# Kernel optimization log

Measured on AMD Instinct MI355X. Metric: run time of the kernel, lower is better.

## Reference

```python
import jax, jax.numpy as jnp
from jax import lax
import numpy as np

ALPHA, BETA, DECAY, GAMMA = 0.9, 0.1, 0.9, 0.5
KW = 5  # temporal_window


def setup_inputs() -> dict:
    key = jax.random.key(0)
    k1, k2 = jax.random.split(key)
    B, T, F = 128, 128, 2048
    x = jax.random.normal(k1, (B, T, F), dtype=jnp.float32)
    init_threshold = jnp.array(1.0, dtype=jnp.float32)
    conv_w = jax.random.normal(k2, (1, 1, KW), dtype=jnp.float32) * 0.2  # Conv1d(1,1,KW) weight
    conv_b = jnp.zeros((1,), dtype=jnp.float32)
    spatial_attn = jnp.array([1.0], dtype=jnp.float32)
    return {"x": x, "init_threshold": init_threshold, "conv_w": conv_w,
            "conv_b": conv_b, "spatial_attn": spatial_attn}


def _forward(x, init_threshold, conv_w, conv_b, spatial_attn):
    B, T, F = x.shape
    # --- temporal encoding: Conv1d(1,1,KW,'same') along time, per (batch,feature) ---
    xt = jnp.transpose(x, (0, 2, 1)).reshape(B * F, 1, T)  # [B*F,1,T]
    conv = lax.conv_general_dilated(xt, conv_w, window_strides=(1,), padding='SAME',
                                    dimension_numbers=('NCH', 'OIH', 'NCH'))
    conv = conv + conv_b[None, :, None]
    x = jnp.transpose(conv.reshape(B, F, T), (0, 2, 1))  # [B,T,F]
    # --- spatial attention ---
    w = jax.nn.sigmoid(spatial_attn * x.mean(axis=1, keepdims=True))  # [B,1,F]
    x = x * (1.0 + GAMMA * w)
    # --- LIF recurrence over time ---
    mem0 = jnp.zeros((B, F), dtype=x.dtype)
    thr0 = jnp.broadcast_to(init_threshold, (B, F)).astype(x.dtype)
    hist0 = jnp.zeros((B, 3, F), dtype=x.dtype)
    pi = jnp.float32(np.pi)

    def step(carry, xt):
        mem, thr, hist = carry
        mem = DECAY * mem + xt
        spike = 0.5 * (jnp.arctan(pi * (mem - thr) / 2) / pi + 0.5)  # multi_atan surrogate
        hist = jnp.concatenate([hist[:, 1:], spike[:, None]], axis=1)  # [B,3,F]
        avg = hist.mean(axis=1)  # [B,F]
        new_thr = ALPHA * thr + (1.0 - ALPHA) * init_threshold + BETA * avg
        mem = mem - spike * lax.stop_gradient(new_thr)
        return (mem, new_thr, hist), spike

    (mem, _, _), spikes = lax.scan(step, (mem0, thr0, hist0), jnp.transpose(x, (1, 0, 2)))
    return jnp.transpose(spikes, (1, 0, 2)), mem  # [B,T,F], [B,F]


def reference(x, init_threshold, conv_w, conv_b, spatial_attn):
    return _forward(x, init_threshold, conv_w, conv_b, spatial_attn)
```

## Files before the change

### kernel.cpp

```cpp
#include <hip/hip_runtime.h>
#include <math.h>

constexpr int B = 128, T = 128, F = 2048, KW = 5;
#define ALPHA 0.9f
#define BETA  0.1f
#define DECAY 0.9f
#define GAMMA 0.5f

typedef float v2f __attribute__((ext_vector_type(2)));

__global__ __launch_bounds__(256, 2) void lif_fused_kernel(
    const float* __restrict__ x,
    const float* __restrict__ thr0p,
    const float* __restrict__ convw,
    const float* __restrict__ convb,
    const float* __restrict__ sattn,
    float* __restrict__ out)
{
    const int tid   = blockIdx.x * blockDim.x + threadIdx.x;
    const int fpair = tid & (F / 2 - 1);
    const int b     = tid >> 10;
    const int f     = fpair * 2;

    const float w0 = convw[0], w1 = convw[1], w2 = convw[2],
                w3 = convw[3], w4 = convw[4];
    const float cb   = convb[0];
    const float thr0 = thr0p[0];
    const float sa   = sattn[0];

    const float* xp = x + (size_t)b * T * F + f;

    v2f s0 = {0.f,0.f}, s1 = {0.f,0.f}, s2 = {0.f,0.f}, s3 = {0.f,0.f},
        s4 = {0.f,0.f}, s5 = {0.f,0.f}, s6 = {0.f,0.f}, s7 = {0.f,0.f};
#pragma unroll 2
    for (int t = 0; t < T; t += 8) {
        v2f v0 = *(const v2f*)(xp + (size_t)(t + 0) * F);
        v2f v1 = *(const v2f*)(xp + (size_t)(t + 1) * F);
        v2f v2 = *(const v2f*)(xp + (size_t)(t + 2) * F);
        v2f v3 = *(const v2f*)(xp + (size_t)(t + 3) * F);
        v2f v4 = *(const v2f*)(xp + (size_t)(t + 4) * F);
        v2f v5 = *(const v2f*)(xp + (size_t)(t + 5) * F);
        v2f v6 = *(const v2f*)(xp + (size_t)(t + 6) * F);
        v2f v7 = *(const v2f*)(xp + (size_t)(t + 7) * F);
        s0 += v0; s1 += v1; s2 += v2; s3 += v3;
        s4 += v4; s5 += v5; s6 += v6; s7 += v7;
    }
    v2f sx = ((s0 + s1) + (s2 + s3)) + ((s4 + s5) + (s6 + s7));

    v2f e0  = *(const v2f*)(xp);
    v2f e1  = *(const v2f*)(xp + (size_t)F);
    v2f em2 = *(const v2f*)(xp + (size_t)(T - 2) * F);
    v2f em1 = *(const v2f*)(xp + (size_t)(T - 1) * F);

    const float W = ((w0 + w1) + (w2 + w3)) + w4;
    v2f csum;
    csum.x = fmaf(W, sx.x, (float)T * cb)
           - (w3 + w4) * e0.x - w4 * e1.x - w0 * em2.x - (w0 + w1) * em1.x;
    csum.y = fmaf(W, sx.y, (float)T * cb)
           - (w3 + w4) * e0.y - w4 * e1.y - w0 * em2.y - (w0 + w1) * em1.y;

    v2f scale;
    {
        float zx = sa * (csum.x * (1.0f / (float)T));
        float zy = sa * (csum.y * (1.0f / (float)T));
        scale.x = 1.0f + GAMMA * (1.0f / (1.0f + expf(-zx)));
        scale.y = 1.0f + GAMMA * (1.0f / (1.0f + expf(-zy)));
    }

    const float PI  = 3.14159265358979323846f;
    const float thc = (1.0f - ALPHA) * thr0;

    v2f mem = {0.f, 0.f};
    v2f thr = {thr0, thr0};
    v2f h1 = {0.f, 0.f}, h2 = {0.f, 0.f};
    v2f a = {0.f, 0.f}, bb = {0.f, 0.f}, c = e0, d = e1;

    float* sp = out + (size_t)b * T * F + f;
    float* mp = out + (size_t)B * T * F + (size_t)b * F + f;

    auto lif_step = [&](int t, v2f e) {
        float cx = fmaf(w0, a.x, fmaf(w1, bb.x, fmaf(w2, c.x,
                   fmaf(w3, d.x, fmaf(w4, e.x, cb)))));
        float cy = fmaf(w0, a.y, fmaf(w1, bb.y, fmaf(w2, c.y,
                   fmaf(w3, d.y, fmaf(w4, e.y, cb)))));
        mem.x = fmaf(DECAY, mem.x, cx * scale.x);
        mem.y = fmaf(DECAY, mem.y, cy * scale.y);
        float sgx = PI * (mem.x - thr.x) * 0.5f;
        float sgy = PI * (mem.y - thr.y) * 0.5f;
        float spx = 0.5f * (atanf(sgx) * (1.0f / PI) + 0.5f);
        float spy = 0.5f * (atanf(sgy) * (1.0f / PI) + 0.5f);
        float avx = (h1.x + h2.x + spx) * (1.0f / 3.0f);
        float avy = (h1.y + h2.y + spy) * (1.0f / 3.0f);
        h1 = h2; h2.x = spx; h2.y = spy;
        thr.x = fmaf(ALPHA, thr.x, fmaf(BETA, avx, thc));
        thr.y = fmaf(ALPHA, thr.y, fmaf(BETA, avy, thc));
        mem.x = fmaf(-spx, thr.x, mem.x);
        mem.y = fmaf(-spy, thr.y, mem.y);
        v2f spv = {spx, spy};
        __builtin_nontemporal_store(spv, (v2f*)(sp + (size_t)t * F));
        a = bb; bb = c; c = d; d = e;
    };

    v2f A[8], Bv[8];

#define LOADG(buf, base)                                        \
    _Pragma("unroll")                                           \
    for (int j = 0; j < 8; ++j)                                 \
        buf[j] = *(const v2f*)(xp + (size_t)((base) + j) * F);

#define COMPUTE8(buf, t0)                                       \
    _Pragma("unroll")                                           \
    for (int j = 0; j < 8; ++j)                                 \
        lif_step((t0) + j, buf[j]);

    LOADG(A, 2);
    for (int p = 0; p < 7; ++p) {
        const int t0 = 16 * p;
        LOADG(Bv, t0 + 10);
        COMPUTE8(A, t0);
        LOADG(A, t0 + 18);
        COMPUTE8(Bv, t0 + 8);
    }
#pragma unroll
    for (int j = 0; j < 8; ++j) {
        if (j < 6) Bv[j] = *(const v2f*)(xp + (size_t)(122 + j) * F);
        else       Bv[j] = (v2f){0.f, 0.f};
    }
    COMPUTE8(A, 112);
    COMPUTE8(Bv, 120);

#undef LOADG
#undef COMPUTE8

    __builtin_nontemporal_store(mem, (v2f*)mp);
}

extern "C" void kernel_launch(void* const* d_in, const int* in_sizes, int n_in,
                              void* d_out, int out_size, void* d_ws, size_t ws_size,
                              hipStream_t stream) {
    const float* x     = (const float*)d_in[0];
    const float* thr0  = (const float*)d_in[1];
    const float* convw = (const float*)d_in[2];
    const float* convb = (const float*)d_in[3];
    const float* sattn = (const float*)d_in[4];
    float* out = (float*)d_out;

    const int total = B * F / 2;
    const int block = 256;
    const int grid  = total / block;

    lif_fused_kernel<<<grid, block, 0, stream>>>(x, thr0, convw, convb, sattn, out);
}
```

Baseline: 251.9 us.

## Use polynomial atan, XCD-aware block mapping, and a simpler time loop

```diff
diff --git a/kernel.cpp b/kernel.cpp
--- a/kernel.cpp
+++ b/kernel.cpp
@@ -9,7 +9,23 @@
 
 typedef float v2f __attribute__((ext_vector_type(2)));
 
-__global__ __launch_bounds__(256, 2) void lif_fused_kernel(
+__device__ __forceinline__ float atan_fast(float z) {
+    float az  = __builtin_fabsf(z);
+    float inv = __builtin_amdgcn_rcpf(az);
+    bool  big = az > 1.0f;
+    float u   = big ? inv : az;
+    float u2  = u * u;
+    float p   = fmaf(u2, -0.01172120f, 0.05265332f);
+    p = fmaf(u2, p, -0.11643287f);
+    p = fmaf(u2, p,  0.19354346f);
+    p = fmaf(u2, p, -0.33262347f);
+    p = fmaf(u2, p,  0.99997726f);
+    float r = u * p;
+    r = big ? (1.57079632679f - r) : r;
+    return copysignf(r, z);
+}
+
+__global__ __launch_bounds__(256) void lif_fused_kernel(
     const float* __restrict__ x,
     const float* __restrict__ thr0p,
     const float* __restrict__ convw,
@@ -17,10 +33,12 @@
     const float* __restrict__ sattn,
     float* __restrict__ out)
 {
-    const int tid   = blockIdx.x * blockDim.x + threadIdx.x;
-    const int fpair = tid & (F / 2 - 1);
-    const int b     = tid >> 10;
-    const int f     = fpair * 2;
+    const int raw    = blockIdx.x;
+    const int xcd    = raw & 7;
+    const int slot   = raw >> 3;
+    const int b      = xcd * 16 + (slot >> 2);
+    const int fchunk = slot & 3;
+    const int f      = fchunk * 512 + (int)threadIdx.x * 2;
 
     const float w0 = convw[0], w1 = convw[1], w2 = convw[2],
                 w3 = convw[3], w4 = convw[4];
@@ -67,8 +85,9 @@
         scale.y = 1.0f + GAMMA * (1.0f / (1.0f + expf(-zy)));
     }
 
-    const float PI  = 3.14159265358979323846f;
-    const float thc = (1.0f - ALPHA) * thr0;
+    const float PIH    = 1.57079632679f;
+    const float INV2PI = 0.15915494309f;
+    const float thc    = (1.0f - ALPHA) * thr0;
 
     v2f mem = {0.f, 0.f};
     v2f thr = {thr0, thr0};
@@ -85,10 +104,8 @@
                    fmaf(w3, d.y, fmaf(w4, e.y, cb)))));
         mem.x = fmaf(DECAY, mem.x, cx * scale.x);
         mem.y = fmaf(DECAY, mem.y, cy * scale.y);
-        float sgx = PI * (mem.x - thr.x) * 0.5f;
-        float sgy = PI * (mem.y - thr.y) * 0.5f;
-        float spx = 0.5f * (atanf(sgx) * (1.0f / PI) + 0.5f);
-        float spy = 0.5f * (atanf(sgy) * (1.0f / PI) + 0.5f);
+        float spx = fmaf(atan_fast(PIH * (mem.x - thr.x)), INV2PI, 0.25f);
+        float spy = fmaf(atan_fast(PIH * (mem.y - thr.y)), INV2PI, 0.25f);
         float avx = (h1.x + h2.x + spx) * (1.0f / 3.0f);
         float avy = (h1.y + h2.y + spy) * (1.0f / 3.0f);
         h1 = h2; h2.x = spx; h2.y = spy;
@@ -101,36 +118,13 @@
         a = bb; bb = c; c = d; d = e;
     };
 
-    v2f A[8], Bv[8];
-
-#define LOADG(buf, base)                                        \
-    _Pragma("unroll")                                           \
-    for (int j = 0; j < 8; ++j)                                 \
-        buf[j] = *(const v2f*)(xp + (size_t)((base) + j) * F);
-
-#define COMPUTE8(buf, t0)                                       \
-    _Pragma("unroll")                                           \
-    for (int j = 0; j < 8; ++j)                                 \
-        lif_step((t0) + j, buf[j]);
-
-    LOADG(A, 2);
-    for (int p = 0; p < 7; ++p) {
-        const int t0 = 16 * p;
-        LOADG(Bv, t0 + 10);
-        COMPUTE8(A, t0);
-        LOADG(A, t0 + 18);
-        COMPUTE8(Bv, t0 + 8);
+#pragma unroll 8
+    for (int t = 0; t < T - 2; ++t) {
+        v2f e = *(const v2f*)(xp + (size_t)(t + 2) * F);
+        lif_step(t, e);
     }
-#pragma unroll
-    for (int j = 0; j < 8; ++j) {
-        if (j < 6) Bv[j] = *(const v2f*)(xp + (size_t)(122 + j) * F);
-        else       Bv[j] = (v2f){0.f, 0.f};
-    }
-    COMPUTE8(A, 112);
-    COMPUTE8(Bv, 120);
-
-#undef LOADG
-#undef COMPUTE8
+    lif_step(T - 2, (v2f){0.f, 0.f});
+    lif_step(T - 1, (v2f){0.f, 0.f});
 
     __builtin_nontemporal_store(mem, (v2f*)mp);
 }
```

After: 252.1 us. Within noise of the previous version (+0.1%).
